# Kernel optimization log

Hardware: AMD Instinct MI355X
Metric: run time of the kernel (lower is better)

Reference implementation:

```python
import jax, jax.numpy as jnp
import numpy as np

HIDDEN_DIM = 256
N = 8192


def setup_inputs() -> dict:
    key = jax.random.key(0)
    k1, k2, k3, k4 = jax.random.split(key, 4)
    img = jax.random.normal(k1, (N, HIDDEN_DIM), dtype=jnp.float32)
    text = jax.random.normal(k2, (N, HIDDEN_DIM), dtype=jnp.float32)
    # nn.Linear(hidden_dim, hidden_dim, bias=False) weights, shape [out, in]
    scale = 1.0 / np.sqrt(HIDDEN_DIM)
    Wq = jax.random.uniform(k3, (HIDDEN_DIM, HIDDEN_DIM), dtype=jnp.float32, minval=-scale, maxval=scale)
    Wk = jax.random.uniform(k4, (HIDDEN_DIM, HIDDEN_DIM), dtype=jnp.float32, minval=-scale, maxval=scale)
    return {"img": img, "text": text, "Wq": Wq, "Wk": Wk}


def reference(img, text, Wq, Wk):
    d = img.shape[-1]
    norm_fact = 1.0 / jnp.sqrt(jnp.asarray(d, dtype=img.dtype))
    Q = img @ Wq.T                       # [N, D]
    K = text @ Wk.T                      # [N, D]
    scores = Q @ K.T                     # [N, N]
    # softmax over dim=1 (keys), then scaled by 1/sqrt(D)
    attn = jax.nn.softmax(scores, axis=1) * norm_fact
    out_img = attn @ img                 # [N, D]
    out_text = attn @ text               # [N, D]
    return (out_img, out_text)
```

## Files before the change

### kernel.cpp

```cpp
#include <hip/hip_runtime.h>

typedef unsigned short ushort_t;
typedef unsigned int uint_t;
typedef __attribute__((ext_vector_type(8))) short short8;
typedef __attribute__((ext_vector_type(8))) _Float16 half8;
typedef __attribute__((ext_vector_type(4))) _Float16 half4;
typedef __attribute__((ext_vector_type(4))) float float4v;

#define MFMA_BF16(a, b, c) __builtin_amdgcn_mfma_f32_16x16x32_bf16((a), (b), (c), 0, 0, 0)
#define MFMA_F16(a, b, c) __builtin_amdgcn_mfma_f32_16x16x32_f16((a), (b), (c), 0, 0, 0)

#define NQ 8192
#define DIM 256
#define DV 512

__device__ __forceinline__ ushort_t f2bf(float x) {
  union { float f; uint_t u; } v; v.f = x;
  return (ushort_t)((v.u + 0x7fffu + ((v.u >> 16) & 1u)) >> 16);
}
__device__ __forceinline__ float bf2f(ushort_t b) {
  union { uint_t u; float f; } v; v.u = ((uint_t)b) << 16;
  return v.f;
}

__device__ __forceinline__ half8 cvt8h(const float* p) {
  float4v a = *(const float4v*)p;
  float4v b = *(const float4v*)(p + 4);
  half8 r;
  r[0] = (_Float16)a[0]; r[1] = (_Float16)a[1];
  r[2] = (_Float16)a[2]; r[3] = (_Float16)a[3];
  r[4] = (_Float16)b[0]; r[5] = (_Float16)b[1];
  r[6] = (_Float16)b[2]; r[7] = (_Float16)b[3];
  return r;
}

__device__ __forceinline__ half8 as_h8(short8 s) {
  union { short8 s; half8 h; } u; u.s = s; return u.h;
}

__device__ __forceinline__ void load_lds_16(const void* g, void* l) {
  __builtin_amdgcn_global_load_lds(
      (const __attribute__((address_space(1))) uint_t*)g,
      (__attribute__((address_space(3))) uint_t*)l, 16, 0, 0);
}

__device__ __forceinline__ void barrier_vm0_lgkm0() {
  asm volatile("s_waitcnt vmcnt(0) lgkmcnt(0)\ns_barrier" ::: "memory");
}
__device__ __forceinline__ void barrier_lgkm0() {
  asm volatile("s_waitcnt lgkmcnt(0)\ns_barrier" ::: "memory");
}

__global__ __launch_bounds__(256, 2) void pre_kernel(
    const float* __restrict__ img, const float* __restrict__ text,
    const float* __restrict__ Wq, const float* __restrict__ Wk,
    _Float16* __restrict__ Qh, _Float16* __restrict__ Kh,
    ushort_t* __restrict__ Vt) {
  __shared__ float tile[64][65];
  const int bid = blockIdx.x;
  const int tid = threadIdx.x;
  if (bid < 1024) {
    const int bx = bid & 127;
    const int by = (bid >> 7) & 3;
    const int bz = bid >> 9;
    const int lane = tid & 63;
    const int wv = tid >> 6;
    const int l16 = lane & 15;
    const int quad = lane >> 4;
    const float* A = bz ? text : img;
    const float* W = bz ? Wk : Wq;
    _Float16* C = bz ? Kh : Qh;
    const int row = bx * 64 + wv * 16 + l16;
    const int colbase = by * 64;

    float4v acc[4];
#pragma unroll
    for (int c = 0; c < 4; ++c) acc[c] = (float4v){0.f, 0.f, 0.f, 0.f};
#pragma unroll
    for (int f = 0; f < 8; ++f) {
      const int k0 = f * 32 + quad * 8;
      half8 af = cvt8h(A + (size_t)row * DIM + k0);
#pragma unroll
      for (int c = 0; c < 4; ++c) {
        half8 bfr = cvt8h(W + (size_t)(colbase + c * 16 + l16) * DIM + k0);
        acc[c] = MFMA_F16(af, bfr, acc[c]);
      }
    }
    const int rbase = bx * 64 + wv * 16 + quad * 4;
#pragma unroll
    for (int c = 0; c < 4; ++c)
#pragma unroll
      for (int r = 0; r < 4; ++r)
        C[(size_t)(rbase + r) * DIM + colbase + c * 16 + l16] = (_Float16)acc[c][r];
  } else {
    const int vb = bid - 1024;
    const int n0 = (vb & 127) * 64;
    const int c0 = (vb >> 7) * 64;
    const float* src = (c0 < 256) ? img : text;
    const int cc0 = (c0 < 256) ? c0 : (c0 - 256);
#pragma unroll
    for (int i = 0; i < 4; ++i) {
      const int r = i * 16 + (tid >> 4);
      const int c = (tid & 15) * 4;
      *(float4v*)&tile[r][c] = *(const float4v*)(src + (size_t)(n0 + r) * DIM + cc0 + c);
    }
    __syncthreads();
    const int c = tid >> 2;
    const int seg = tid & 3;
    ushort_t tmp[16];
#pragma unroll
    for (int t = 0; t < 16; ++t) tmp[t] = f2bf(tile[seg * 16 + t][c]);
    ushort_t* dst = Vt + (size_t)(c0 + c) * NQ + n0 + seg * 16;
    *(short8*)dst = *(short8*)&tmp[0];
    *(short8*)(dst + 8) = *(short8*)&tmp[8];
  }
}

__device__ __forceinline__ void stage_K(const _Float16* __restrict__ Kh, int k0,
                                        ushort_t* dst, int tid, int wv) {
#pragma unroll
  for (int i = 0; i < 4; ++i) {
    const int chunk = i * 256 + tid;
    const int n = chunk >> 5;
    const int cs = (chunk & 31) ^ (n & 7);
    load_lds_16(Kh + (size_t)(k0 + n) * DIM + cs * 8,
                (char*)dst + (i * 256 + wv * 64) * 16);
  }
}

__global__ __launch_bounds__(256, 2) void attn_kernel(
    const _Float16* __restrict__ Qh, const _Float16* __restrict__ Kh,
    const ushort_t* __restrict__ Vt, _Float16* __restrict__ pacc,
    float* __restrict__ pdenom, int kps, int ks) {
  extern __shared__ __align__(16) ushort_t smem[];

  const int tid = threadIdx.x;
  const int lane = tid & 63;
  const int wv = tid >> 6;
  const int l16 = lane & 15;
  const int quad = lane >> 4;
  const int id = blockIdx.x;
  const int split = id & (ks - 1);
  const int qtile = id / ks;
  const int kbeg = split * kps;
  const int sw2 = (l16 >> 1) & 3;
  const int swk = l16 & 7;

  short8 qf[8];
  {
    const _Float16* qptr = Qh + (size_t)(qtile * 64 + wv * 16 + l16) * DIM;
#pragma unroll
    for (int f = 0; f < 8; ++f)
      qf[f] = *(const short8*)(qptr + f * 32 + quad * 8);
  }

  float4v acc[4][8];
#pragma unroll
  for (int m = 0; m < 4; ++m)
#pragma unroll
    for (int c = 0; c < 8; ++c) acc[m][c] = (float4v){0.f, 0.f, 0.f, 0.f};
  float dacc[4] = {0.f, 0.f, 0.f, 0.f};

  const int ntiles = kps >> 5;

  stage_K(Kh, kbeg, smem, tid, wv);

  for (int t = 0; t < ntiles; ++t) {
    const ushort_t* Kt = smem + (t & 1) * 8192;
    barrier_vm0_lgkm0();

    float4v s0 = (float4v){0.f, 0.f, 0.f, 0.f};
    float4v s1 = (float4v){0.f, 0.f, 0.f, 0.f};

    if (t > 0) {
      const ushort_t* Vg = Vt + (size_t)(kbeg + (t - 1) * 32 + quad * 8);
      short8 vb[8];
#pragma unroll
      for (int p = 0; p < 3; ++p)
        vb[p] = *(const short8*)(Vg + (size_t)((wv * 8 + p) * 16 + l16) * NQ);
      if (t + 1 < ntiles)
        stage_K(Kh, kbeg + (t + 1) * 32, smem + ((t + 1) & 1) * 8192, tid, wv);
      const ushort_t* Pprev = smem + 16384 + ((t - 1) & 1) * 2048;
      short8 pa[4];
#pragma unroll
      for (int m = 0; m < 4; ++m)
        pa[m] = *(const short8*)(Pprev + (m * 16 + l16) * 32 + (quad ^ sw2) * 8);
#pragma unroll
      for (int c = 0; c < 8; ++c) {
        if (c + 3 < 8)
          vb[c + 3] = *(const short8*)(Vg + (size_t)((wv * 8 + c + 3) * 16 + l16) * NQ);
        const int cs = ((c * 4 + quad) ^ swk) * 8;
        short8 kb0 = *(const short8*)(Kt + l16 * DIM + cs);
        short8 kb1 = *(const short8*)(Kt + (l16 + 16) * DIM + cs);
        s0 = MFMA_F16(as_h8(qf[c]), as_h8(kb0), s0);
        s1 = MFMA_F16(as_h8(qf[c]), as_h8(kb1), s1);
#pragma unroll
        for (int m = 0; m < 4; ++m)
          acc[m][c] = MFMA_BF16(pa[m], vb[c], acc[m][c]);
      }
    } else {
      if (t + 1 < ntiles)
        stage_K(Kh, kbeg + (t + 1) * 32, smem + ((t + 1) & 1) * 8192, tid, wv);
#pragma unroll
      for (int f = 0; f < 8; ++f) {
        const int cs = ((f * 4 + quad) ^ swk) * 8;
        short8 kb0 = *(const short8*)(Kt + l16 * DIM + cs);
        short8 kb1 = *(const short8*)(Kt + (l16 + 16) * DIM + cs);
        s0 = MFMA_F16(as_h8(qf[f]), as_h8(kb0), s0);
        s1 = MFMA_F16(as_h8(qf[f]), as_h8(kb1), s1);
      }
    }

    ushort_t* Pcur = smem + 16384 + (t & 1) * 2048;
    ushort_t pb0[4], pb1[4];
#pragma unroll
    for (int r = 0; r < 4; ++r) {
      pb0[r] = f2bf(__expf(s0[r]));
      pb1[r] = f2bf(__expf(s1[r]));
    }
#pragma unroll
    for (int r = 0; r < 4; ++r) {
      const int rb = wv * 16 + quad * 4 + r;
      const int swp = (rb >> 1) & 3;
      Pcur[rb * 32 + ((l16 >> 3) ^ swp) * 8 + (l16 & 7)] = pb0[r];
      Pcur[rb * 32 + ((2 + (l16 >> 3)) ^ swp) * 8 + (l16 & 7)] = pb1[r];
    }
#pragma unroll
    for (int r = 0; r < 4; ++r) {
      float ts = bf2f(pb0[r]) + bf2f(pb1[r]);
      ts += __shfl_xor(ts, 1);
      ts += __shfl_xor(ts, 2);
      ts += __shfl_xor(ts, 4);
      ts += __shfl_xor(ts, 8);
      dacc[r] += ts;
    }
  }

  barrier_vm0_lgkm0();
  {
    const ushort_t* Pprev = smem + 16384 + ((ntiles - 1) & 1) * 2048;
    const ushort_t* Vg = Vt + (size_t)(kbeg + (ntiles - 1) * 32 + quad * 8);
    short8 pa[4];
#pragma unroll
    for (int m = 0; m < 4; ++m)
      pa[m] = *(const short8*)(Pprev + (m * 16 + l16) * 32 + (quad ^ sw2) * 8);
#pragma unroll
    for (int c = 0; c < 8; ++c) {
      const int vcol = (wv * 8 + c) * 16 + l16;
      short8 vb = *(const short8*)(Vg + (size_t)vcol * NQ);
#pragma unroll
      for (int m = 0; m < 4; ++m)
        acc[m][c] = MFMA_BF16(pa[m], vb, acc[m][c]);
    }
  }

  barrier_lgkm0();
  float* ldsD = (float*)smem;
  if (l16 == 0) {
#pragma unroll
    for (int r = 0; r < 4; ++r)
      ldsD[wv * 16 + quad * 4 + r] = dacc[r];
  }
  barrier_lgkm0();

  _Float16* pout = pacc + (size_t)split * ((size_t)NQ * DV);
#pragma unroll
  for (int m = 0; m < 4; ++m) {
    float invd[4];
#pragma unroll
    for (int r = 0; r < 4; ++r) invd[r] = 1.0f / ldsD[m * 16 + quad * 4 + r];
    const int rowbase = qtile * 64 + m * 16 + quad * 4;
#pragma unroll
    for (int c = 0; c < 8; ++c) {
      const int col = (wv * 8 + c) * 16 + l16;
#pragma unroll
      for (int r = 0; r < 4; ++r)
        pout[(size_t)(rowbase + r) * DV + col] = (_Float16)(acc[m][c][r] * invd[r]);
    }
  }
  if (l16 == 0) {
    const int rowbase = qtile * 64 + wv * 16 + quad * 4;
#pragma unroll
    for (int r = 0; r < 4; ++r)
      pdenom[split * NQ + rowbase + r] = dacc[r];
  }
}

__global__ __launch_bounds__(256) void combine_kernel(
    const _Float16* __restrict__ pacc, const float* __restrict__ pdenom,
    float* __restrict__ out, int ks) {
  const int idx = blockIdx.x * 256 + threadIdx.x;
  const int n = idx >> 7;
  const int c4 = (idx & 127) << 2;
  float4v s = (float4v){0.f, 0.f, 0.f, 0.f};
  float dsum = 0.f;
  for (int sp = 0; sp < ks; ++sp) {
    const float d = pdenom[sp * NQ + n];
    half4 x = *(const half4*)(pacc + (size_t)sp * ((size_t)NQ * DV) + (size_t)n * DV + c4);
    s[0] += d * (float)x[0];
    s[1] += d * (float)x[1];
    s[2] += d * (float)x[2];
    s[3] += d * (float)x[3];
    dsum += d;
  }
  const float scale = 1.0f / (16.0f * dsum);
  s *= scale;
  float* dst = (c4 < 256) ? (out + (size_t)n * DIM + c4)
                          : (out + (size_t)NQ * DIM + (size_t)n * DIM + (c4 - 256));
  *(float4v*)dst = s;
}

extern "C" void kernel_launch(void* const* d_in, const int* in_sizes, int n_in,
                              void* d_out, int out_size, void* d_ws, size_t ws_size,
                              hipStream_t stream) {
  const float* img = (const float*)d_in[0];
  const float* text = (const float*)d_in[1];
  const float* Wq = (const float*)d_in[2];
  const float* Wk = (const float*)d_in[3];
  float* out = (float*)d_out;
  char* ws = (char*)d_ws;

  _Float16* Qh = (_Float16*)ws;
  _Float16* Kh = (_Float16*)(ws + ((size_t)4 << 20));
  ushort_t* Vt = (ushort_t*)(ws + ((size_t)8 << 20));
  const size_t accsz = (size_t)NQ * DV * sizeof(_Float16);
  const size_t base = (size_t)16 << 20;

  int ks = 4;
  if (ws_size < base + 4 * (accsz + NQ * sizeof(float))) ks = 2;
  _Float16* pacc = (_Float16*)(ws + base);
  float* pdenom = (float*)(ws + base + (size_t)ks * accsz);

  hipLaunchKernelGGL(pre_kernel, dim3(2048), dim3(256), 0, stream,
                     img, text, Wq, Wk, Qh, Kh, Vt);
  hipLaunchKernelGGL(attn_kernel, dim3(128 * ks), dim3(256),
                     20480 * sizeof(ushort_t), stream,
                     Qh, Kh, Vt, pacc, pdenom, NQ / ks, ks);
  hipLaunchKernelGGL(combine_kernel, dim3((NQ * DV / 4) / 256), dim3(256), 0, stream,
                     pacc, pdenom, out, ks);
}
```

Baseline: 272.6 us.

## Prefetch V across iterations, raise MFMA priority, defer row-sum shuffles

Issues the first three V-fragment global loads for the next tile at the end of the current iteration, so their latency overlaps the softmax and P-store work. The next-K staging is moved to right after the barrier, and the MFMA loop runs at raised wave priority. The per-tile cross-lane shuffle reduction of row sums is replaced by per-lane accumulation, with a single shuffle reduction after the loop. Carrying the prefetched V values across iterations raises register pressure, and per-lane partial sums slightly change the summation order.

New measurement: 288.3 us. +5.7%, slower.

```diff
diff --git a/kernel.cpp b/kernel.cpp
--- a/kernel.cpp
+++ b/kernel.cpp
@@ -165,29 +165,30 @@
 
   stage_K(Kh, kbeg, smem, tid, wv);
 
+  short8 vp0, vp1, vp2;
+
   for (int t = 0; t < ntiles; ++t) {
     const ushort_t* Kt = smem + (t & 1) * 8192;
     barrier_vm0_lgkm0();
+    if (t + 1 < ntiles)
+      stage_K(Kh, kbeg + (t + 1) * 32, smem + ((t + 1) & 1) * 8192, tid, wv);
 
     float4v s0 = (float4v){0.f, 0.f, 0.f, 0.f};
     float4v s1 = (float4v){0.f, 0.f, 0.f, 0.f};
 
     if (t > 0) {
+      const ushort_t* Pprev = smem + 16384 + ((t - 1) & 1) * 2048;
       const ushort_t* Vg = Vt + (size_t)(kbeg + (t - 1) * 32 + quad * 8);
-      short8 vb[8];
-#pragma unroll
-      for (int p = 0; p < 3; ++p)
-        vb[p] = *(const short8*)(Vg + (size_t)((wv * 8 + p) * 16 + l16) * NQ);
-      if (t + 1 < ntiles)
-        stage_K(Kh, kbeg + (t + 1) * 32, smem + ((t + 1) & 1) * 8192, tid, wv);
-      const ushort_t* Pprev = smem + 16384 + ((t - 1) & 1) * 2048;
       short8 pa[4];
 #pragma unroll
       for (int m = 0; m < 4; ++m)
         pa[m] = *(const short8*)(Pprev + (m * 16 + l16) * 32 + (quad ^ sw2) * 8);
+      short8 vb[8];
+      vb[0] = vp0; vb[1] = vp1; vb[2] = vp2;
+      __builtin_amdgcn_s_setprio(1);
 #pragma unroll
       for (int c = 0; c < 8; ++c) {
-        if (c + 3 < 8)
+        if (c < 5)
           vb[c + 3] = *(const short8*)(Vg + (size_t)((wv * 8 + c + 3) * 16 + l16) * NQ);
         const int cs = ((c * 4 + quad) ^ swk) * 8;
         short8 kb0 = *(const short8*)(Kt + l16 * DIM + cs);
@@ -198,9 +199,8 @@
         for (int m = 0; m < 4; ++m)
           acc[m][c] = MFMA_BF16(pa[m], vb[c], acc[m][c]);
       }
+      __builtin_amdgcn_s_setprio(0);
     } else {
-      if (t + 1 < ntiles)
-        stage_K(Kh, kbeg + (t + 1) * 32, smem + ((t + 1) & 1) * 8192, tid, wv);
 #pragma unroll
       for (int f = 0; f < 8; ++f) {
         const int cs = ((f * 4 + quad) ^ swk) * 8;
@@ -211,6 +211,13 @@
       }
     }
 
+    {
+      const ushort_t* Vnx = Vt + (size_t)(kbeg + t * 32 + quad * 8);
+      vp0 = *(const short8*)(Vnx + (size_t)((wv * 8 + 0) * 16 + l16) * NQ);
+      vp1 = *(const short8*)(Vnx + (size_t)((wv * 8 + 1) * 16 + l16) * NQ);
+      vp2 = *(const short8*)(Vnx + (size_t)((wv * 8 + 2) * 16 + l16) * NQ);
+    }
+
     ushort_t* Pcur = smem + 16384 + (t & 1) * 2048;
     ushort_t pb0[4], pb1[4];
 #pragma unroll
@@ -224,15 +231,7 @@
       const int swp = (rb >> 1) & 3;
       Pcur[rb * 32 + ((l16 >> 3) ^ swp) * 8 + (l16 & 7)] = pb0[r];
       Pcur[rb * 32 + ((2 + (l16 >> 3)) ^ swp) * 8 + (l16 & 7)] = pb1[r];
-    }
-#pragma unroll
-    for (int r = 0; r < 4; ++r) {
-      float ts = bf2f(pb0[r]) + bf2f(pb1[r]);
-      ts += __shfl_xor(ts, 1);
-      ts += __shfl_xor(ts, 2);
-      ts += __shfl_xor(ts, 4);
-      ts += __shfl_xor(ts, 8);
-      dacc[r] += ts;
+      dacc[r] += bf2f(pb0[r]) + bf2f(pb1[r]);
     }
   }
 
@@ -244,14 +243,26 @@
 #pragma unroll
     for (int m = 0; m < 4; ++m)
       pa[m] = *(const short8*)(Pprev + (m * 16 + l16) * 32 + (quad ^ sw2) * 8);
+    short8 vb[8];
+    vb[0] = vp0; vb[1] = vp1; vb[2] = vp2;
 #pragma unroll
     for (int c = 0; c < 8; ++c) {
-      const int vcol = (wv * 8 + c) * 16 + l16;
-      short8 vb = *(const short8*)(Vg + (size_t)vcol * NQ);
+      if (c < 5)
+        vb[c + 3] = *(const short8*)(Vg + (size_t)((wv * 8 + c + 3) * 16 + l16) * NQ);
 #pragma unroll
       for (int m = 0; m < 4; ++m)
-        acc[m][c] = MFMA_BF16(pa[m], vb, acc[m][c]);
-    }
+        acc[m][c] = MFMA_BF16(pa[m], vb[c], acc[m][c]);
+    }
+  }
+
+#pragma unroll
+  for (int r = 0; r < 4; ++r) {
+    float ts = dacc[r];
+    ts += __shfl_xor(ts, 1);
+    ts += __shfl_xor(ts, 2);
+    ts += __shfl_xor(ts, 4);
+    ts += __shfl_xor(ts, 8);
+    dacc[r] = ts;
   }
 
   barrier_lgkm0();
```
